# Kernel tuning notes

Hardware: AMD Instinct MI355X
Metric: run time of the kernel (lower is better)

## Reference

```python
import jax, jax.numpy as jnp
import numpy as np

# OpenCV fixed separable Gaussian kernel for ksize=3, sigma=0 (getGaussianKernel small-kernel table)
GAUSS_1D = jnp.array([0.25, 0.5, 0.25], dtype=jnp.float32)
# OpenCV Laplacian kernel for ksize=3 (Sobel dxx + dyy aperture 3)
LAP_K = jnp.array([[2.0, 0.0, 2.0], [0.0, -8.0, 0.0], [2.0, 0.0, 2.0]], dtype=jnp.float32)


def _depthwise_conv(img, kernel2d):
    # img: (N, H, W); kernel2d: (kh, kw). BORDER_REFLECT_101 == jnp.pad mode='reflect'.
    kh, kw = kernel2d.shape
    ph, pw = kh // 2, kw // 2
    padded = jnp.pad(img, ((0, 0), (ph, ph), (pw, pw)), mode='reflect')
    out = jax.lax.conv_general_dilated(
        padded[:, None, :, :], kernel2d[None, None, :, :],
        window_strides=(1, 1), padding='VALID')
    return out[:, 0]


def setup_inputs() -> dict:
    key = jax.random.key(0)
    x = jax.random.uniform(key, (32, 3, 512, 512), dtype=jnp.float32)
    return {"x": x}


def reference(x):
    B, C, H, W = x.shape
    img = x.reshape(B * C, H, W)
    # src = clip(x*255, 0, 255).astype('uint8')  -> truncation toward zero (values >= 0, so floor)
    src = jnp.floor(jnp.clip(img * 255.0, 0.0, 255.0))
    # cv2.GaussianBlur(ksize=3, sigma=0): separable [1,2,1]/4 kernel, rounded back to uint8
    g2d = GAUSS_1D[:, None] * GAUSS_1D[None, :]
    blurred = jnp.clip(jnp.round(_depthwise_conv(src, g2d)), 0.0, 255.0)
    # cv2.Laplacian(CV_16S, ksize=3): integer-exact on integer-valued input
    lap = _depthwise_conv(blurred, LAP_K)
    # cv2.convertScaleAbs: saturate_cast<uchar>(|dst|)
    abs_dst = jnp.clip(jnp.round(jnp.abs(lap)), 0.0, 255.0)
    return abs_dst.reshape(B, C, H, W)
```

## Files before the change

kernel.cpp:

```cpp
#include <hip/hip_runtime.h>
#include <math.h>

#define IMG_H 512
#define IMG_W 512
#define TW 256
#define TH 32
#define SRC_ROWS 36
#define SRC_SLOTS 66

typedef float f32x4 __attribute__((ext_vector_type(4)));

__device__ __forceinline__ int reflect101(int i, int n) {
    if (i < 0) i = -i;
    if (i >= n) i = 2 * n - 2 - i;
    return i;
}

__device__ __forceinline__ unsigned int quant4(float4 v) {
    unsigned int a = (unsigned int)(v.x * 255.0f);
    unsigned int b = (unsigned int)(v.y * 255.0f);
    unsigned int c = (unsigned int)(v.z * 255.0f);
    unsigned int d = (unsigned int)(v.w * 255.0f);
    return a | (b << 8) | (c << 16) | (d << 24);
}

#define LOADR(k, RA, RB) do {                                                 \
    RA = *(const uint2*)&s_src[lr0 + (k)][sb];                                \
    RB = *(const uint2*)&s_src[lr0 + (k)][sb + 2];                            \
} while (0)

#define UNPK(RA, RB, Q) do {                                                  \
    Q##0  = (float)((RA.x >> 16) & 0xffu);                                    \
    Q##1  = (float)(RA.x >> 24);                                              \
    Q##2  = (float)(RA.y & 0xffu);                                            \
    Q##3  = (float)((RA.y >> 8) & 0xffu);                                     \
    Q##4  = (float)((RA.y >> 16) & 0xffu);                                    \
    Q##5  = (float)(RA.y >> 24);                                              \
    Q##6  = (float)(RB.x & 0xffu);                                            \
    Q##7  = (float)((RB.x >> 8) & 0xffu);                                     \
    Q##8  = (float)((RB.x >> 16) & 0xffu);                                    \
    Q##9  = (float)(RB.x >> 24);                                              \
    Q##10 = (float)(RB.y & 0xffu);                                            \
    Q##11 = (float)((RB.y >> 8) & 0xffu);                                     \
} while (0)

#define EMAKE(E, QA, QB) do {                                                 \
    E##0 = QA##0 + QB##0;   E##1 = QA##1 + QB##1;                             \
    E##2 = QA##2 + QB##2;   E##3 = QA##3 + QB##3;                             \
    E##4 = QA##4 + QB##4;   E##5 = QA##5 + QB##5;                             \
    E##6 = QA##6 + QB##6;   E##7 = QA##7 + QB##7;                             \
    E##8 = QA##8 + QB##8;   E##9 = QA##9 + QB##9;                             \
    E##10 = QA##10 + QB##10; E##11 = QA##11 + QB##11;                         \
} while (0)

#define BLMAKE(BL, EA, EB) do {                                               \
    float cs0 = EA##0 + EB##0,   cs1 = EA##1 + EB##1;                         \
    float cs2 = EA##2 + EB##2,   cs3 = EA##3 + EB##3;                         \
    float cs4 = EA##4 + EB##4,   cs5 = EA##5 + EB##5;                         \
    float cs6 = EA##6 + EB##6,   cs7 = EA##7 + EB##7;                         \
    float cs8 = EA##8 + EB##8,   cs9 = EA##9 + EB##9;                         \
    float cs10 = EA##10 + EB##10, cs11 = EA##11 + EB##11;                     \
    float d0 = cs0 + cs1, d1 = cs1 + cs2, d2 = cs2 + cs3, d3 = cs3 + cs4;     \
    float d4 = cs4 + cs5, d5 = cs5 + cs6, d6 = cs6 + cs7, d7 = cs7 + cs8;     \
    float d8 = cs8 + cs9, d9 = cs9 + cs10, d10 = cs10 + cs11;                 \
    BL##0 = rintf((d0 + d1) * 0.0625f);                                       \
    BL##1 = rintf((d1 + d2) * 0.0625f);                                       \
    BL##2 = rintf((d2 + d3) * 0.0625f);                                       \
    BL##3 = rintf((d3 + d4) * 0.0625f);                                       \
    BL##4 = rintf((d4 + d5) * 0.0625f);                                       \
    BL##5 = rintf((d5 + d6) * 0.0625f);                                       \
    BL##6 = rintf((d6 + d7) * 0.0625f);                                       \
    BL##7 = rintf((d7 + d8) * 0.0625f);                                       \
    BL##8 = rintf((d8 + d9) * 0.0625f);                                       \
    BL##9 = rintf((d9 + d10) * 0.0625f);                                      \
} while (0)

#define OUTROW(BA, BB, BC, T) do {                                            \
    float u0 = BA##0 + BC##0, u1 = BA##1 + BC##1, u2 = BA##2 + BC##2;         \
    float u3 = BA##3 + BC##3, u4 = BA##4 + BC##4, u5 = BA##5 + BC##5;         \
    float u6 = BA##6 + BC##6, u7 = BA##7 + BC##7, u8 = BA##8 + BC##8;         \
    float u9 = BA##9 + BC##9;                                                 \
    f32x4 oA_, oB_;                                                           \
    float h_;                                                                 \
    h_ = fmaf(-4.0f, BB##1, u0 + u2); oA_.x = fminf(2.0f * fabsf(h_), 255.0f);\
    h_ = fmaf(-4.0f, BB##2, u1 + u3); oA_.y = fminf(2.0f * fabsf(h_), 255.0f);\
    h_ = fmaf(-4.0f, BB##3, u2 + u4); oA_.z = fminf(2.0f * fabsf(h_), 255.0f);\
    h_ = fmaf(-4.0f, BB##4, u3 + u5); oA_.w = fminf(2.0f * fabsf(h_), 255.0f);\
    h_ = fmaf(-4.0f, BB##5, u4 + u6); oB_.x = fminf(2.0f * fabsf(h_), 255.0f);\
    h_ = fmaf(-4.0f, BB##6, u5 + u7); oB_.y = fminf(2.0f * fabsf(h_), 255.0f);\
    h_ = fmaf(-4.0f, BB##7, u6 + u8); oB_.z = fminf(2.0f * fabsf(h_), 255.0f);\
    h_ = fmaf(-4.0f, BB##8, u7 + u9); oB_.w = fminf(2.0f * fabsf(h_), 255.0f);\
    float* orow_ = &op[(size_t)(ty0 + yb + (T)) * IMG_W + xo];                \
    *(f32x4*)orow_ = oA_;                                                     \
    *(f32x4*)(orow_ + 4) = oB_;                                               \
} while (0)

__global__ __launch_bounds__(256, 8) void lap_fused(const float* __restrict__ in,
                                                    float* __restrict__ out) {
    __shared__ unsigned int s_src[SRC_ROWS][SRC_SLOTS];

    const int img = blockIdx.z;
    const int ty0 = blockIdx.y * TH;
    const int tx0 = blockIdx.x * TW;
    const float* __restrict__ ip = in + (size_t)img * (IMG_H * IMG_W);
    float* __restrict__ op = out + (size_t)img * (IMG_H * IMG_W);
    const int tid = threadIdx.x;

    {
        const int j = 1 + (tid & 63);
        const int r0 = tid >> 6;
        const int gx0 = tx0 - 4 + 4 * j;
        #pragma unroll
        for (int k = 0; k < 9; ++k) {
            int r = r0 + 4 * k;
            int gy = reflect101(ty0 + r - 2, IMG_H);
            float4 v = *(const float4*)(ip + (size_t)gy * IMG_W + gx0);
            s_src[r][j] = quant4(v);
        }
    }
    if (tid < 72) {
        int r = tid >> 1;
        int j = (tid & 1) * 65;
        int gy = reflect101(ty0 + r - 2, IMG_H);
        int gx0 = tx0 - 4 + 4 * j;
        const float* rowp = ip + (size_t)gy * IMG_W;
        float4 v;
        float* pv = (float*)&v;
        #pragma unroll
        for (int k = 0; k < 4; ++k) pv[k] = rowp[reflect101(gx0 + k, IMG_W)];
        s_src[r][j] = quant4(v);
    }
    __syncthreads();

    const int cg = tid & 31;
    const int rb = tid >> 5;
    const int xo = tx0 + 8 * cg;
    const int sb = 2 * cg;
    const int lr0 = 4 * rb;
    const int yb = 4 * rb;

    uint2 r0a, r0b, r1a, r1b, r2a, r2b, r3a, r3b;
    uint2 r4a, r4b, r5a, r5b, r6a, r6b, r7a, r7b;
    float qA0, qA1, qA2, qA3, qA4, qA5, qA6, qA7, qA8, qA9, qA10, qA11;
    float qB0, qB1, qB2, qB3, qB4, qB5, qB6, qB7, qB8, qB9, qB10, qB11;
    float eA0, eA1, eA2, eA3, eA4, eA5, eA6, eA7, eA8, eA9, eA10, eA11;
    float eB0, eB1, eB2, eB3, eB4, eB5, eB6, eB7, eB8, eB9, eB10, eB11;
    float bP0, bP1, bP2, bP3, bP4, bP5, bP6, bP7, bP8, bP9;
    float bQ0, bQ1, bQ2, bQ3, bQ4, bQ5, bQ6, bQ7, bQ8, bQ9;
    float bR0, bR1, bR2, bR3, bR4, bR5, bR6, bR7, bR8, bR9;

    LOADR(0, r0a, r0b); LOADR(1, r1a, r1b); LOADR(2, r2a, r2b); LOADR(3, r3a, r3b);
    UNPK(r0a, r0b, qA);
    UNPK(r1a, r1b, qB);  EMAKE(eA, qA, qB);
    LOADR(4, r4a, r4b);
    UNPK(r2a, r2b, qA);  EMAKE(eB, qB, qA);  BLMAKE(bP, eA, eB);
    LOADR(5, r5a, r5b);
    UNPK(r3a, r3b, qB);  EMAKE(eA, qA, qB);  BLMAKE(bQ, eB, eA);
    LOADR(6, r6a, r6b);
    UNPK(r4a, r4b, qA);  EMAKE(eB, qB, qA);  BLMAKE(bR, eA, eB);
    OUTROW(bP, bQ, bR, 0);
    LOADR(7, r7a, r7b);
    UNPK(r5a, r5b, qB);  EMAKE(eA, qA, qB);  BLMAKE(bP, eB, eA);
    OUTROW(bQ, bR, bP, 1);
    UNPK(r6a, r6b, qA);  EMAKE(eB, qB, qA);  BLMAKE(bQ, eA, eB);
    OUTROW(bR, bP, bQ, 2);
    UNPK(r7a, r7b, qB);  EMAKE(eA, qA, qB);  BLMAKE(bR, eB, eA);
    OUTROW(bP, bQ, bR, 3);
}

extern "C" void kernel_launch(void* const* d_in, const int* in_sizes, int n_in,
                              void* d_out, int out_size, void* d_ws, size_t ws_size,
                              hipStream_t stream) {
    const float* x = (const float*)d_in[0];
    float* out = (float*)d_out;
    dim3 grid(IMG_W / TW, IMG_H / TH, 96);
    dim3 block(256);
    lap_fused<<<grid, block, 0, stream>>>(x, out);
}
```

Before: 43.61 us.

## Process two row tiles per block with double-buffered prefetch

Each block now handles two vertically adjacent 32-row tiles. It issues the global loads for the second tile before computing the first, so memory latency overlaps with compute, and it keeps the two quantized tiles in a double-buffered shared array. The grid is halved and the launch-bounds occupancy hint drops from 8 to 4, trading fewer resident blocks for more in-flight loads per block. Per block the halo rows fall from 36 of 32 to 72 of 64, since each tile still loads its own halo.

New measurement: 40.58 us. -6.9%, faster.

```diff
diff --git a/kernel.cpp b/kernel.cpp
--- a/kernel.cpp
+++ b/kernel.cpp
@@ -24,9 +24,32 @@
     return a | (b << 8) | (c << 16) | (d << 24);
 }
 
-#define LOADR(k, RA, RB) do {                                                 \
-    RA = *(const uint2*)&s_src[lr0 + (k)][sb];                                \
-    RB = *(const uint2*)&s_src[lr0 + (k)][sb + 2];                            \
+#define ISSUE_TILE(TYB, VV, EE) do {                                          \
+    _Pragma("unroll")                                                         \
+    for (int k_ = 0; k_ < 9; ++k_) {                                          \
+        int r_ = r0s + 4 * k_;                                                \
+        int gy_ = reflect101((TYB) + r_ - 2, IMG_H);                          \
+        VV[k_] = *(const float4*)(ip + (size_t)gy_ * IMG_W + gxs);            \
+    }                                                                         \
+    if (tid < 72) {                                                           \
+        int gy_ = reflect101((TYB) + (tid >> 1) - 2, IMG_H);                  \
+        const float* rowp_ = ip + (size_t)gy_ * IMG_W;                        \
+        float* pe_ = (float*)&EE;                                             \
+        _Pragma("unroll")                                                     \
+        for (int k2_ = 0; k2_ < 4; ++k2_)                                     \
+            pe_[k2_] = rowp_[reflect101(gxe + k2_, IMG_W)];                   \
+    }                                                                         \
+} while (0)
+
+#define PACK_TILE(S, VV, EE) do {                                             \
+    _Pragma("unroll")                                                         \
+    for (int k_ = 0; k_ < 9; ++k_) s_src[S][r0s + 4 * k_][js] = quant4(VV[k_]);\
+    if (tid < 72) s_src[S][tid >> 1][je] = quant4(EE);                        \
+} while (0)
+
+#define LOADR(S, k, RA, RB) do {                                              \
+    RA = *(const uint2*)&s_src[S][lr0 + (k)][sb];                             \
+    RB = *(const uint2*)&s_src[S][lr0 + (k)][sb + 2];                         \
 } while (0)
 
 #define UNPK(RA, RB, Q) do {                                                  \
@@ -75,7 +98,7 @@
     BL##9 = rintf((d9 + d10) * 0.0625f);                                      \
 } while (0)
 
-#define OUTROW(BA, BB, BC, T) do {                                            \
+#define OUTROW(BA, BB, BC, T, OB) do {                                        \
     float u0 = BA##0 + BC##0, u1 = BA##1 + BC##1, u2 = BA##2 + BC##2;         \
     float u3 = BA##3 + BC##3, u4 = BA##4 + BC##4, u5 = BA##5 + BC##5;         \
     float u6 = BA##6 + BC##6, u7 = BA##7 + BC##7, u8 = BA##8 + BC##8;         \
@@ -90,47 +113,57 @@
     h_ = fmaf(-4.0f, BB##6, u5 + u7); oB_.y = fminf(2.0f * fabsf(h_), 255.0f);\
     h_ = fmaf(-4.0f, BB##7, u6 + u8); oB_.z = fminf(2.0f * fabsf(h_), 255.0f);\
     h_ = fmaf(-4.0f, BB##8, u7 + u9); oB_.w = fminf(2.0f * fabsf(h_), 255.0f);\
-    float* orow_ = &op[(size_t)(ty0 + yb + (T)) * IMG_W + xo];                \
+    float* orow_ = &op[(size_t)((OB) + yb + (T)) * IMG_W + xo];               \
     *(f32x4*)orow_ = oA_;                                                     \
     *(f32x4*)(orow_ + 4) = oB_;                                               \
 } while (0)
 
-__global__ __launch_bounds__(256, 8) void lap_fused(const float* __restrict__ in,
+#define COMPUTE_TILE(S, OB) do {                                              \
+    uint2 r0a, r0b, r1a, r1b, r2a, r2b, r3a, r3b;                             \
+    uint2 r4a, r4b, r5a, r5b, r6a, r6b, r7a, r7b;                             \
+    float qA0, qA1, qA2, qA3, qA4, qA5, qA6, qA7, qA8, qA9, qA10, qA11;       \
+    float qB0, qB1, qB2, qB3, qB4, qB5, qB6, qB7, qB8, qB9, qB10, qB11;       \
+    float eA0, eA1, eA2, eA3, eA4, eA5, eA6, eA7, eA8, eA9, eA10, eA11;       \
+    float eB0, eB1, eB2, eB3, eB4, eB5, eB6, eB7, eB8, eB9, eB10, eB11;       \
+    float bP0, bP1, bP2, bP3, bP4, bP5, bP6, bP7, bP8, bP9;                   \
+    float bQ0, bQ1, bQ2, bQ3, bQ4, bQ5, bQ6, bQ7, bQ8, bQ9;                   \
+    float bR0, bR1, bR2, bR3, bR4, bR5, bR6, bR7, bR8, bR9;                   \
+    LOADR(S, 0, r0a, r0b); LOADR(S, 1, r1a, r1b);                             \
+    LOADR(S, 2, r2a, r2b); LOADR(S, 3, r3a, r3b);                             \
+    UNPK(r0a, r0b, qA);                                                       \
+    UNPK(r1a, r1b, qB);  EMAKE(eA, qA, qB);                                   \
+    LOADR(S, 4, r4a, r4b);                                                    \
+    UNPK(r2a, r2b, qA);  EMAKE(eB, qB, qA);  BLMAKE(bP, eA, eB);              \
+    LOADR(S, 5, r5a, r5b);                                                    \
+    UNPK(r3a, r3b, qB);  EMAKE(eA, qA, qB);  BLMAKE(bQ, eB, eA);              \
+    LOADR(S, 6, r6a, r6b);                                                    \
+    UNPK(r4a, r4b, qA);  EMAKE(eB, qB, qA);  BLMAKE(bR, eA, eB);              \
+    OUTROW(bP, bQ, bR, 0, OB);                                                \
+    LOADR(S, 7, r7a, r7b);                                                    \
+    UNPK(r5a, r5b, qB);  EMAKE(eA, qA, qB);  BLMAKE(bP, eB, eA);              \
+    OUTROW(bQ, bR, bP, 1, OB);                                                \
+    UNPK(r6a, r6b, qA);  EMAKE(eB, qB, qA);  BLMAKE(bQ, eA, eB);              \
+    OUTROW(bR, bP, bQ, 2, OB);                                                \
+    UNPK(r7a, r7b, qB);  EMAKE(eA, qA, qB);  BLMAKE(bR, eB, eA);              \
+    OUTROW(bP, bQ, bR, 3, OB);                                                \
+} while (0)
+
+__global__ __launch_bounds__(256, 4) void lap_fused(const float* __restrict__ in,
                                                     float* __restrict__ out) {
-    __shared__ unsigned int s_src[SRC_ROWS][SRC_SLOTS];
+    __shared__ unsigned int s_src[2][SRC_ROWS][SRC_SLOTS];
 
     const int img = blockIdx.z;
-    const int ty0 = blockIdx.y * TH;
+    const int ty0 = blockIdx.y * (2 * TH);
     const int tx0 = blockIdx.x * TW;
     const float* __restrict__ ip = in + (size_t)img * (IMG_H * IMG_W);
     float* __restrict__ op = out + (size_t)img * (IMG_H * IMG_W);
     const int tid = threadIdx.x;
 
-    {
-        const int j = 1 + (tid & 63);
-        const int r0 = tid >> 6;
-        const int gx0 = tx0 - 4 + 4 * j;
-        #pragma unroll
-        for (int k = 0; k < 9; ++k) {
-            int r = r0 + 4 * k;
-            int gy = reflect101(ty0 + r - 2, IMG_H);
-            float4 v = *(const float4*)(ip + (size_t)gy * IMG_W + gx0);
-            s_src[r][j] = quant4(v);
-        }
-    }
-    if (tid < 72) {
-        int r = tid >> 1;
-        int j = (tid & 1) * 65;
-        int gy = reflect101(ty0 + r - 2, IMG_H);
-        int gx0 = tx0 - 4 + 4 * j;
-        const float* rowp = ip + (size_t)gy * IMG_W;
-        float4 v;
-        float* pv = (float*)&v;
-        #pragma unroll
-        for (int k = 0; k < 4; ++k) pv[k] = rowp[reflect101(gx0 + k, IMG_W)];
-        s_src[r][j] = quant4(v);
-    }
-    __syncthreads();
+    const int js = 1 + (tid & 63);
+    const int r0s = tid >> 6;
+    const int gxs = tx0 - 4 + 4 * js;
+    const int je = (tid & 1) * 65;
+    const int gxe = tx0 - 4 + 4 * je;
 
     const int cg = tid & 31;
     const int rb = tid >> 5;
@@ -139,33 +172,19 @@
     const int lr0 = 4 * rb;
     const int yb = 4 * rb;
 
-    uint2 r0a, r0b, r1a, r1b, r2a, r2b, r3a, r3b;
-    uint2 r4a, r4b, r5a, r5b, r6a, r6b, r7a, r7b;
-    float qA0, qA1, qA2, qA3, qA4, qA5, qA6, qA7, qA8, qA9, qA10, qA11;
-    float qB0, qB1, qB2, qB3, qB4, qB5, qB6, qB7, qB8, qB9, qB10, qB11;
-    float eA0, eA1, eA2, eA3, eA4, eA5, eA6, eA7, eA8, eA9, eA10, eA11;
-    float eB0, eB1, eB2, eB3, eB4, eB5, eB6, eB7, eB8, eB9, eB10, eB11;
-    float bP0, bP1, bP2, bP3, bP4, bP5, bP6, bP7, bP8, bP9;
-    float bQ0, bQ1, bQ2, bQ3, bQ4, bQ5, bQ6, bQ7, bQ8, bQ9;
-    float bR0, bR1, bR2, bR3, bR4, bR5, bR6, bR7, bR8, bR9;
+    float4 vv[9];
+    float4 ee;
 
-    LOADR(0, r0a, r0b); LOADR(1, r1a, r1b); LOADR(2, r2a, r2b); LOADR(3, r3a, r3b);
-    UNPK(r0a, r0b, qA);
-    UNPK(r1a, r1b, qB);  EMAKE(eA, qA, qB);
-    LOADR(4, r4a, r4b);
-    UNPK(r2a, r2b, qA);  EMAKE(eB, qB, qA);  BLMAKE(bP, eA, eB);
-    LOADR(5, r5a, r5b);
-    UNPK(r3a, r3b, qB);  EMAKE(eA, qA, qB);  BLMAKE(bQ, eB, eA);
-    LOADR(6, r6a, r6b);
-    UNPK(r4a, r4b, qA);  EMAKE(eB, qB, qA);  BLMAKE(bR, eA, eB);
-    OUTROW(bP, bQ, bR, 0);
-    LOADR(7, r7a, r7b);
-    UNPK(r5a, r5b, qB);  EMAKE(eA, qA, qB);  BLMAKE(bP, eB, eA);
-    OUTROW(bQ, bR, bP, 1);
-    UNPK(r6a, r6b, qA);  EMAKE(eB, qB, qA);  BLMAKE(bQ, eA, eB);
-    OUTROW(bR, bP, bQ, 2);
-    UNPK(r7a, r7b, qB);  EMAKE(eA, qA, qB);  BLMAKE(bR, eB, eA);
-    OUTROW(bP, bQ, bR, 3);
+    ISSUE_TILE(ty0, vv, ee);
+    PACK_TILE(0, vv, ee);
+    __syncthreads();
+
+    ISSUE_TILE(ty0 + TH, vv, ee);
+    COMPUTE_TILE(0, ty0);
+    PACK_TILE(1, vv, ee);
+    __syncthreads();
+
+    COMPUTE_TILE(1, ty0 + TH);
 }
 
 extern "C" void kernel_launch(void* const* d_in, const int* in_sizes, int n_in,
@@ -173,7 +192,7 @@
                               hipStream_t stream) {
     const float* x = (const float*)d_in[0];
     float* out = (float*)d_out;
-    dim3 grid(IMG_W / TW, IMG_H / TH, 96);
+    dim3 grid(IMG_W / TW, IMG_H / (2 * TH), 96);
     dim3 block(256);
     lap_fused<<<grid, block, 0, stream>>>(x, out);
 }
```

## Drop shared-memory staging; load and quantize halo rows directly from global

Applied to the files above, without the earlier changes.

Removes the shared-memory tile, its cooperative quantize-and-pack load and the __syncthreads. Each thread now reads its own 8 rows of 16 floats (including halo) directly from global memory, with branchless reflect handling at the image edges, and quantizes them in registers. Launch bounds drop from 8 to 4 blocks per SM to allow more registers. The aim is to eliminate the barrier and LDS traffic at the cost of redundant global/L2 reads of the halo rows and columns, plus lower occupancy.

Measured after the change: 53.98 us. 23.8% more time.

```diff
diff --git a/kernel.cpp b/kernel.cpp
--- a/kernel.cpp
+++ b/kernel.cpp
@@ -3,10 +3,6 @@
 
 #define IMG_H 512
 #define IMG_W 512
-#define TW 256
-#define TH 32
-#define SRC_ROWS 36
-#define SRC_SLOTS 66
 
 typedef float f32x4 __attribute__((ext_vector_type(4)));
 
@@ -16,32 +12,29 @@
     return i;
 }
 
-__device__ __forceinline__ unsigned int quant4(float4 v) {
-    unsigned int a = (unsigned int)(v.x * 255.0f);
-    unsigned int b = (unsigned int)(v.y * 255.0f);
-    unsigned int c = (unsigned int)(v.z * 255.0f);
-    unsigned int d = (unsigned int)(v.w * 255.0f);
-    return a | (b << 8) | (c << 16) | (d << 24);
-}
-
-#define LOADR(k, RA, RB) do {                                                 \
-    RA = *(const uint2*)&s_src[lr0 + (k)][sb];                                \
-    RB = *(const uint2*)&s_src[lr0 + (k)][sb + 2];                            \
+#define LOADROW(RY, A, B, C, D) do {                                          \
+    const float* rp_ = ip + (size_t)reflect101((RY), IMG_H) * IMG_W;          \
+    A = *(const f32x4*)(rp_ + b0);                                            \
+    B = *(const f32x4*)(rp_ + b1);                                            \
+    C = *(const f32x4*)(rp_ + b2);                                            \
+    D = *(const f32x4*)(rp_ + b3);                                            \
 } while (0)
 
-#define UNPK(RA, RB, Q) do {                                                  \
-    Q##0  = (float)((RA.x >> 16) & 0xffu);                                    \
-    Q##1  = (float)(RA.x >> 24);                                              \
-    Q##2  = (float)(RA.y & 0xffu);                                            \
-    Q##3  = (float)((RA.y >> 8) & 0xffu);                                     \
-    Q##4  = (float)((RA.y >> 16) & 0xffu);                                    \
-    Q##5  = (float)(RA.y >> 24);                                              \
-    Q##6  = (float)(RB.x & 0xffu);                                            \
-    Q##7  = (float)((RB.x >> 8) & 0xffu);                                     \
-    Q##8  = (float)((RB.x >> 16) & 0xffu);                                    \
-    Q##9  = (float)(RB.x >> 24);                                              \
-    Q##10 = (float)(RB.y & 0xffu);                                            \
-    Q##11 = (float)((RB.y >> 8) & 0xffu);                                     \
+#define QROW(A, B, C, D, Q) do {                                              \
+    float m1_ = le ? A.y : A.w;                                               \
+    float c8_ = re ? D.z : D.x;                                               \
+    Q##0  = floorf(A.z * 255.0f);                                             \
+    Q##1  = floorf(m1_ * 255.0f);                                             \
+    Q##2  = floorf(B.x * 255.0f);                                             \
+    Q##3  = floorf(B.y * 255.0f);                                             \
+    Q##4  = floorf(B.z * 255.0f);                                             \
+    Q##5  = floorf(B.w * 255.0f);                                             \
+    Q##6  = floorf(C.x * 255.0f);                                             \
+    Q##7  = floorf(C.y * 255.0f);                                             \
+    Q##8  = floorf(C.z * 255.0f);                                             \
+    Q##9  = floorf(C.w * 255.0f);                                             \
+    Q##10 = floorf(c8_ * 255.0f);                                             \
+    Q##11 = floorf(D.y * 255.0f);                                             \
 } while (0)
 
 #define EMAKE(E, QA, QB) do {                                                 \
@@ -90,81 +83,60 @@
     h_ = fmaf(-4.0f, BB##6, u5 + u7); oB_.y = fminf(2.0f * fabsf(h_), 255.0f);\
     h_ = fmaf(-4.0f, BB##7, u6 + u8); oB_.z = fminf(2.0f * fabsf(h_), 255.0f);\
     h_ = fmaf(-4.0f, BB##8, u7 + u9); oB_.w = fminf(2.0f * fabsf(h_), 255.0f);\
-    float* orow_ = &op[(size_t)(ty0 + yb + (T)) * IMG_W + xo];                \
+    float* orow_ = &op[(size_t)(yb + (T)) * IMG_W + xo];                      \
     *(f32x4*)orow_ = oA_;                                                     \
     *(f32x4*)(orow_ + 4) = oB_;                                               \
 } while (0)
 
-__global__ __launch_bounds__(256, 8) void lap_fused(const float* __restrict__ in,
+__global__ __launch_bounds__(256, 4) void lap_fused(const float* __restrict__ in,
                                                     float* __restrict__ out) {
-    __shared__ unsigned int s_src[SRC_ROWS][SRC_SLOTS];
-
     const int img = blockIdx.z;
-    const int ty0 = blockIdx.y * TH;
-    const int tx0 = blockIdx.x * TW;
     const float* __restrict__ ip = in + (size_t)img * (IMG_H * IMG_W);
     float* __restrict__ op = out + (size_t)img * (IMG_H * IMG_W);
     const int tid = threadIdx.x;
 
-    {
-        const int j = 1 + (tid & 63);
-        const int r0 = tid >> 6;
-        const int gx0 = tx0 - 4 + 4 * j;
-        #pragma unroll
-        for (int k = 0; k < 9; ++k) {
-            int r = r0 + 4 * k;
-            int gy = reflect101(ty0 + r - 2, IMG_H);
-            float4 v = *(const float4*)(ip + (size_t)gy * IMG_W + gx0);
-            s_src[r][j] = quant4(v);
-        }
-    }
-    if (tid < 72) {
-        int r = tid >> 1;
-        int j = (tid & 1) * 65;
-        int gy = reflect101(ty0 + r - 2, IMG_H);
-        int gx0 = tx0 - 4 + 4 * j;
-        const float* rowp = ip + (size_t)gy * IMG_W;
-        float4 v;
-        float* pv = (float*)&v;
-        #pragma unroll
-        for (int k = 0; k < 4; ++k) pv[k] = rowp[reflect101(gx0 + k, IMG_W)];
-        s_src[r][j] = quant4(v);
-    }
-    __syncthreads();
-
     const int cg = tid & 31;
     const int rb = tid >> 5;
-    const int xo = tx0 + 8 * cg;
-    const int sb = 2 * cg;
-    const int lr0 = 4 * rb;
-    const int yb = 4 * rb;
+    const int xo = blockIdx.x * 256 + 8 * cg;
+    const int yb = blockIdx.y * 32 + 4 * rb;
 
-    uint2 r0a, r0b, r1a, r1b, r2a, r2b, r3a, r3b;
-    uint2 r4a, r4b, r5a, r5b, r6a, r6b, r7a, r7b;
+    const int b0 = (xo == 0) ? 0 : (xo - 4);
+    const int b1 = xo;
+    const int b2 = xo + 4;
+    const int b3 = (xo + 8 > IMG_W - 4) ? (IMG_W - 4) : (xo + 8);
+    const bool le = (xo == 0);
+    const bool re = (xo + 8 > IMG_W - 4);
+
+    f32x4 A0, B0, C0, D0, A1, B1, C1, D1;
     float qA0, qA1, qA2, qA3, qA4, qA5, qA6, qA7, qA8, qA9, qA10, qA11;
     float qB0, qB1, qB2, qB3, qB4, qB5, qB6, qB7, qB8, qB9, qB10, qB11;
+    float qC0, qC1, qC2, qC3, qC4, qC5, qC6, qC7, qC8, qC9, qC10, qC11;
     float eA0, eA1, eA2, eA3, eA4, eA5, eA6, eA7, eA8, eA9, eA10, eA11;
     float eB0, eB1, eB2, eB3, eB4, eB5, eB6, eB7, eB8, eB9, eB10, eB11;
     float bP0, bP1, bP2, bP3, bP4, bP5, bP6, bP7, bP8, bP9;
     float bQ0, bQ1, bQ2, bQ3, bQ4, bQ5, bQ6, bQ7, bQ8, bQ9;
     float bR0, bR1, bR2, bR3, bR4, bR5, bR6, bR7, bR8, bR9;
 
-    LOADR(0, r0a, r0b); LOADR(1, r1a, r1b); LOADR(2, r2a, r2b); LOADR(3, r3a, r3b);
-    UNPK(r0a, r0b, qA);
-    UNPK(r1a, r1b, qB);  EMAKE(eA, qA, qB);
-    LOADR(4, r4a, r4b);
-    UNPK(r2a, r2b, qA);  EMAKE(eB, qB, qA);  BLMAKE(bP, eA, eB);
-    LOADR(5, r5a, r5b);
-    UNPK(r3a, r3b, qB);  EMAKE(eA, qA, qB);  BLMAKE(bQ, eB, eA);
-    LOADR(6, r6a, r6b);
-    UNPK(r4a, r4b, qA);  EMAKE(eB, qB, qA);  BLMAKE(bR, eA, eB);
+    LOADROW(yb - 2, A0, B0, C0, D0);
+    LOADROW(yb - 1, A1, B1, C1, D1);
+    QROW(A0, B0, C0, D0, qA);  LOADROW(yb + 0, A0, B0, C0, D0);
+    QROW(A1, B1, C1, D1, qB);  LOADROW(yb + 1, A1, B1, C1, D1);
+    EMAKE(eA, qA, qB);
+    QROW(A0, B0, C0, D0, qC);  LOADROW(yb + 2, A0, B0, C0, D0);
+    EMAKE(eB, qB, qC);  BLMAKE(bP, eA, eB);
+    QROW(A1, B1, C1, D1, qA);  LOADROW(yb + 3, A1, B1, C1, D1);
+    EMAKE(eA, qC, qA);  BLMAKE(bQ, eB, eA);
+    QROW(A0, B0, C0, D0, qB);  LOADROW(yb + 4, A0, B0, C0, D0);
+    EMAKE(eB, qA, qB);  BLMAKE(bR, eA, eB);
     OUTROW(bP, bQ, bR, 0);
-    LOADR(7, r7a, r7b);
-    UNPK(r5a, r5b, qB);  EMAKE(eA, qA, qB);  BLMAKE(bP, eB, eA);
+    QROW(A1, B1, C1, D1, qC);  LOADROW(yb + 5, A1, B1, C1, D1);
+    EMAKE(eA, qB, qC);  BLMAKE(bP, eB, eA);
     OUTROW(bQ, bR, bP, 1);
-    UNPK(r6a, r6b, qA);  EMAKE(eB, qB, qA);  BLMAKE(bQ, eA, eB);
+    QROW(A0, B0, C0, D0, qA);
+    EMAKE(eB, qC, qA);  BLMAKE(bQ, eA, eB);
     OUTROW(bR, bP, bQ, 2);
-    UNPK(r7a, r7b, qB);  EMAKE(eA, qA, qB);  BLMAKE(bR, eB, eA);
+    QROW(A1, B1, C1, D1, qB);
+    EMAKE(eA, qA, qB);  BLMAKE(bR, eB, eA);
     OUTROW(bP, bQ, bR, 3);
 }
 
@@ -173,7 +145,7 @@
                               hipStream_t stream) {
     const float* x = (const float*)d_in[0];
     float* out = (float*)d_out;
-    dim3 grid(IMG_W / TW, IMG_H / TH, 96);
+    dim3 grid(IMG_W / 256, IMG_H / 32, 96);
     dim3 block(256);
     lap_fused<<<grid, block, 0, stream>>>(x, out);
 }
```
